# Optimization experiments

Hardware: AMD Instinct MI355X
Metric: run time of the kernel (lower is better)

The kernel has to match this reference:

```python
import jax, jax.numpy as jnp
import numpy as np

B, L, T, IN, H, OUT = 1024, 64, 128, 13, 64, 13
NEG = -1e30


def gru_step(x, h, Wih, Whh, bih, bhh):
    # PyTorch GRU cell: gates ordered (r, z, n)
    gi = x @ Wih.T + bih          # [B, 3H]
    gh = h @ Whh.T + bhh          # [B, 3H]
    ir, iz, inn = jnp.split(gi, 3, axis=-1)
    hr, hz, hn = jnp.split(gh, 3, axis=-1)
    r = jax.nn.sigmoid(ir + hr)
    z = jax.nn.sigmoid(iz + hz)
    n = jnp.tanh(inn + r * hn)
    return (1.0 - z) * n + z * h


def setup_inputs() -> dict:
    key = jax.random.key(0)
    ks = jax.random.split(key, 10)
    s = float(1.0 / np.sqrt(H))
    x = jax.random.normal(ks[0], (B, L, IN), jnp.float32)
    lengths = jax.random.randint(ks[1], (B,), 1, L + 1).at[0].set(L)
    Wih = jax.random.uniform(ks[2], (3 * H, IN), jnp.float32, -s, s)
    Whh = jax.random.uniform(ks[3], (3 * H, H), jnp.float32, -s, s)
    bih = jax.random.uniform(ks[4], (3 * H,), jnp.float32, -s, s)
    bhh = jax.random.uniform(ks[5], (3 * H,), jnp.float32, -s, s)
    Wf = jax.random.uniform(ks[6], (OUT, H), jnp.float32, -s, s)
    bf = jax.random.uniform(ks[7], (OUT,), jnp.float32, -s, s)
    Wa = jax.random.uniform(ks[8], (H, H), jnp.float32, -s, s)
    ba = jax.random.uniform(ks[9], (H,), jnp.float32, -s, s)
    return dict(x=x, lengths=lengths, output_length=T, Wih=Wih, Whh=Whh,
                bih=bih, bhh=bhh, Wf=Wf, bf=bf, Wa=Wa, ba=ba)


def reference(x, lengths, output_length, Wih, Whh, bih, bhh, Wf, bf, Wa, ba):
    b, l = x.shape[0], x.shape[1]
    xT = jnp.swapaxes(x, 0, 1)                        # [L, B, IN]
    h0 = jnp.zeros((b, H), x.dtype)

    # Encoder: masked GRU emulating pack_padded/pad_packed semantics:
    # hidden frozen past each sequence's length; outputs zero past length.
    def enc(h, inp):
        t, xt = inp
        hn = gru_step(xt, h, Wih, Whh, bih, bhh)
        valid = (t < lengths)[:, None]
        h = jnp.where(valid, hn, h)
        return h, jnp.where(valid, hn, 0.0)

    h, outs = jax.lax.scan(enc, h0, (jnp.arange(l), xT))
    # output[:, -1, :] of the padded output (zeros for seqs shorter than max)
    nin = outs[-1] @ Wf.T + bf                        # [B, OUT]

    Tn = output_length
    buf0 = jnp.zeros((Tn, b, H), x.dtype)             # growing past-prediction buffer

    def dec(carry, t):
        h, buf, nin = carry
        hn = gru_step(nin, h, Wih, Whh, bih, bhh)     # output_lstm == hidden (1 layer, 1 step)
        # attention recomputed over all past predictions (softmax over time axis)
        logits = jnp.einsum('tbh,gh->tbg', buf, Wa) + ba      # [T, B, H]
        logits = jnp.where((jnp.arange(Tn) < t)[:, None, None], logits, NEG)
        w = jax.nn.softmax(logits, axis=0)
        o = hn + jnp.sum(w * buf, axis=0)             # at t=0 buffer is all zeros -> +0
        y = o @ Wf.T + bf
        return (hn, buf.at[t].set(o), y), y

    _, ys = jax.lax.scan(dec, (h, buf0, nin), jnp.arange(Tn))
    return jnp.swapaxes(ys, 0, 1)                     # [B, T, OUT]
```

## Files before the change

kernel.cpp:

```cpp
#include <hip/hip_runtime.h>
#include <stdint.h>
#include <math.h>

#define BATCH 1024
#define SEQL  64
#define TDEC  128
#define NIN   13
#define NH    64
#define NOUT  13

typedef _Float16 h2 __attribute__((ext_vector_type(2)));
typedef __fp16   g2 __attribute__((ext_vector_type(2)));

union FU  { uint32_t u; float f; };
union HU  { uint16_t u; _Float16 h; };
union H2U { uint32_t u; h2 h; g2 g; };

__device__ __forceinline__ float bf2f(uint16_t v) { FU t; t.u = ((uint32_t)v) << 16; return t.f; }
__device__ __forceinline__ float hf2f(uint16_t v) { HU t; t.u = v; return (float)t.h; }

__device__ __forceinline__ float ldf(const void* p, long i, int mode) {
    if (mode == 1) return bf2f(((const uint16_t*)p)[i]);
    if (mode == 2) return hf2f(((const uint16_t*)p)[i]);
    return ((const float*)p)[i];
}

__device__ __forceinline__ bool pass_stats(const void* p, int n, int lane, int mode,
                                           float band_lo, float band_hi, float max_ok) {
    int m = (n + 1) / 2;
    int cnt = (m < 64) ? m : 64;
    bool ok_max = true, in_band = false;
    if (lane < cnt) {
        long pos = 2L * (((long)lane * m) / cnt);
        float v = (mode == 1) ? bf2f(((const uint16_t*)p)[pos])
                              : hf2f(((const uint16_t*)p)[pos]);
        float a = fabsf(v);
        ok_max  = (a <= max_ok);
        in_band = (a >= band_lo && a <= band_hi);
    }
    bool allmax = __all(ok_max);
    int nb = (int)__popcll(__ballot(in_band));
    int need = cnt / 4; if (need < 1) need = 1;
    return allmax && (nb >= need);
}
__device__ __forceinline__ int detect(const void* p, int n, int lane,
                                      float band_lo, float band_hi, float max_ok) {
    if (pass_stats(p, n, lane, 1, band_lo, band_hi, max_ok)) return 1;
    if (pass_stats(p, n, lane, 2, band_lo, band_hi, max_ok)) return 2;
    return 0;
}
__device__ __forceinline__ bool detect_len64(const int* p, int lane) {
    int v = p[2 * lane + 1];
    return __all(v == 0);
}

__device__ __forceinline__ float dot2(h2 a, h2 b, float c) {
#if __has_builtin(__builtin_amdgcn_fdot2)
    return __builtin_amdgcn_fdot2(a, b, c, false);
#else
    return c + (float)a[0] * (float)b[0] + (float)a[1] * (float)b[1];
#endif
}
__device__ __forceinline__ uint32_t pku(float a, float b) {
    H2U t; t.g = __builtin_amdgcn_cvt_pkrtz(a, b); return t.u;
}
__device__ __forceinline__ h2 uh(uint32_t u) { H2U t; t.u = u; return t.h; }
__device__ __forceinline__ float rcp_(float x) { return __builtin_amdgcn_rcpf(x); }
__device__ __forceinline__ float sigm(float x)  { return rcp_(1.0f + __expf(-x)); }
__device__ __forceinline__ float tanh_(float x) { return 1.0f - 2.0f * rcp_(__expf(2.0f * x) + 1.0f); }
__device__ __forceinline__ void wb() { __builtin_amdgcn_wave_barrier(); }

__global__ __launch_bounds__(64, 1)
void gru_attn_kernel(const void* __restrict__ x, const int* __restrict__ lengths,
                     const void* __restrict__ Wih, const void* __restrict__ Whh,
                     const void* __restrict__ bih, const void* __restrict__ bhh,
                     const void* __restrict__ Wf, const void* __restrict__ bfv,
                     const void* __restrict__ Wa, const void* __restrict__ ba,
                     float* __restrict__ out)
{
    const int b = blockIdx.x;
    const int j = threadIdx.x;

    __shared__ __align__(16) uint32_t xs2[SEQL][8];
    __shared__ __align__(16) uint32_t hs2[NH / 2];
    __shared__ __align__(16) uint32_t os2[NH / 2];
    __shared__ __align__(16) uint32_t xd2[8];

    const int dX   = detect(x,   BATCH * SEQL * NIN, j, 0.25f, 4.0f, 16.0f);
    const int dWih = detect(Wih, 3 * NH * NIN, j, 0.04f, 0.13f, 0.14f);
    const int dWhh = detect(Whh, 3 * NH * NH,  j, 0.04f, 0.13f, 0.14f);
    const int dBih = detect(bih, 3 * NH,       j, 0.04f, 0.13f, 0.14f);
    const int dBhh = detect(bhh, 3 * NH,       j, 0.04f, 0.13f, 0.14f);
    const int dWf  = detect(Wf,  NOUT * NH,    j, 0.04f, 0.13f, 0.14f);
    const int dBf  = detect(bfv, NOUT,         j, 0.04f, 0.13f, 0.14f);
    const int dWa  = detect(Wa,  NH * NH,      j, 0.04f, 0.13f, 0.14f);
    const int dBa  = detect(ba,  NH,           j, 0.04f, 0.13f, 0.14f);
    const bool len64 = detect_len64(lengths, j);

    h2 wihr[7], wihz[7], wihn[7];
    h2 whhr[32], whhz[32], whhn[32];
    h2 wap[32], wfp[32];

#pragma unroll
    for (int k = 0; k < 7; ++k) {
        float a0 = ldf(Wih, (0 * NH + j) * NIN + 2 * k, dWih);
        float a1 = (2 * k + 1 < NIN) ? ldf(Wih, (0 * NH + j) * NIN + 2 * k + 1, dWih) : 0.0f;
        wihr[k] = uh(pku(a0, a1));
        float b0 = ldf(Wih, (1 * NH + j) * NIN + 2 * k, dWih);
        float b1 = (2 * k + 1 < NIN) ? ldf(Wih, (1 * NH + j) * NIN + 2 * k + 1, dWih) : 0.0f;
        wihz[k] = uh(pku(b0, b1));
        float c0 = ldf(Wih, (2 * NH + j) * NIN + 2 * k, dWih);
        float c1 = (2 * k + 1 < NIN) ? ldf(Wih, (2 * NH + j) * NIN + 2 * k + 1, dWih) : 0.0f;
        wihn[k] = uh(pku(c0, c1));
    }
    const int jf = (j < NOUT) ? j : 0;
#pragma unroll
    for (int k = 0; k < 32; ++k) {
        whhr[k] = uh(pku(ldf(Whh, (0 * NH + j) * NH + 2 * k, dWhh),
                         ldf(Whh, (0 * NH + j) * NH + 2 * k + 1, dWhh)));
        whhz[k] = uh(pku(ldf(Whh, (1 * NH + j) * NH + 2 * k, dWhh),
                         ldf(Whh, (1 * NH + j) * NH + 2 * k + 1, dWhh)));
        whhn[k] = uh(pku(ldf(Whh, (2 * NH + j) * NH + 2 * k, dWhh),
                         ldf(Whh, (2 * NH + j) * NH + 2 * k + 1, dWhh)));
        wap[k]  = uh(pku(ldf(Wa, j * NH + 2 * k, dWa),
                         ldf(Wa, j * NH + 2 * k + 1, dWa)));
        wfp[k]  = uh(pku(ldf(Wf, jf * NH + 2 * k, dWf),
                         ldf(Wf, jf * NH + 2 * k + 1, dWf)));
    }

    const float bcr = ldf(bih, j, dBih)          + ldf(bhh, j, dBhh);
    const float bcz = ldf(bih, NH + j, dBih)     + ldf(bhh, NH + j, dBhh);
    const float bni = ldf(bih, 2 * NH + j, dBih);
    const float bnh = ldf(bhh, 2 * NH + j, dBhh);
    const float baj = ldf(ba, j, dBa);
    const float bfj = ldf(bfv, jf, dBf);
    const int len = len64 ? lengths[2 * b] : lengths[b];

    {
        const long base = ((long)b * SEQL + j) * NIN;
        float v[14];
#pragma unroll
        for (int k = 0; k < NIN; ++k) v[k] = ldf(x, base + k, dX);
        v[13] = 0.0f;
#pragma unroll
        for (int p = 0; p < 7; ++p) xs2[j][p] = pku(v[2 * p], v[2 * p + 1]);
        xs2[j][7] = 0u;
    }
    if (j < NH / 2) hs2[j] = 0u;
    if (j == 0) xd2[7] = 0u;
    wb();

    float h = 0.0f;
    float out_last = 0.0f;

    for (int t = 0; t < SEQL; ++t) {
        float ar = bcr, az = bcz, an = bni, hna = bnh;
        {
            const uint32_t* xr = xs2[t];
            uint4 q0 = *(const uint4*)xr;
            uint4 q1 = *(const uint4*)(xr + 4);
            uint32_t xw[8] = {q0.x, q0.y, q0.z, q0.w, q1.x, q1.y, q1.z, q1.w};
#pragma unroll
            for (int p = 0; p < 7; ++p) {
                h2 xv = uh(xw[p]);
                ar = dot2(wihr[p], xv, ar);
                az = dot2(wihz[p], xv, az);
                an = dot2(wihn[p], xv, an);
            }
        }
        float ar2 = 0.0f, az2 = 0.0f, hn2 = 0.0f;
        {
            const uint4* hp = (const uint4*)hs2;
#pragma unroll
            for (int q = 0; q < 8; ++q) {
                uint4 blk = hp[q];
                uint32_t w[4] = {blk.x, blk.y, blk.z, blk.w};
#pragma unroll
                for (int e = 0; e < 4; ++e) {
                    int k = 4 * q + e;
                    h2 hv = uh(w[e]);
                    if (e & 1) { ar2 = dot2(whhr[k], hv, ar2); az2 = dot2(whhz[k], hv, az2); hn2 = dot2(whhn[k], hv, hn2); }
                    else       { ar  = dot2(whhr[k], hv, ar);  az  = dot2(whhz[k], hv, az);  hna = dot2(whhn[k], hv, hna); }
                }
            }
        }
        ar += ar2; az += az2; hna += hn2;
        float r = sigm(ar);
        float z = sigm(az);
        float n = tanh_(an + r * hna);
        float hnew = n + z * (h - n);
        if (t < len) h = hnew;
        if (t == SEQL - 1) out_last = (t < len) ? hnew : 0.0f;
        float hpart = __shfl_xor(h, 1);
        if (!(j & 1)) hs2[j >> 1] = pku(h, hpart);
        wb();
    }

    {
        float opart = __shfl_xor(out_last, 1);
        if (!(j & 1)) os2[j >> 1] = pku(out_last, opart);
        wb();
        float nv = bfj, nv2 = 0.0f;
        const uint4* op = (const uint4*)os2;
#pragma unroll
        for (int q = 0; q < 8; ++q) {
            uint4 blk = op[q];
            uint32_t w[4] = {blk.x, blk.y, blk.z, blk.w};
#pragma unroll
            for (int e = 0; e < 4; ++e) {
                int k = 4 * q + e;
                h2 ov = uh(w[e]);
                if (e & 1) nv2 = dot2(wfp[k], ov, nv2);
                else       nv  = dot2(wfp[k], ov, nv);
            }
        }
        nv += nv2;
        float nz = (j < NOUT) ? nv : 0.0f;
        float np = __shfl_xor(nz, 1);
        if (!(j & 1) && j < 14) xd2[j >> 1] = pku(nz, np);
        wb();
    }

    float m = -1e30f, Zs = 0.0f, num = 0.0f;

    for (int t = 0; t < TDEC; ++t) {
        float ar = bcr, az = bcz, an = bni, hna = bnh;
        {
            uint4 q0 = *(const uint4*)xd2;
            uint4 q1 = *(const uint4*)(xd2 + 4);
            uint32_t xw[8] = {q0.x, q0.y, q0.z, q0.w, q1.x, q1.y, q1.z, q1.w};
#pragma unroll
            for (int p = 0; p < 7; ++p) {
                h2 xv = uh(xw[p]);
                ar = dot2(wihr[p], xv, ar);
                az = dot2(wihz[p], xv, az);
                an = dot2(wihn[p], xv, an);
            }
        }
        float ar2 = 0.0f, az2 = 0.0f, hn2 = 0.0f;
        {
            const uint4* hp = (const uint4*)hs2;
#pragma unroll
            for (int q = 0; q < 8; ++q) {
                uint4 blk = hp[q];
                uint32_t w[4] = {blk.x, blk.y, blk.z, blk.w};
#pragma unroll
                for (int e = 0; e < 4; ++e) {
                    int k = 4 * q + e;
                    h2 hv = uh(w[e]);
                    if (e & 1) { ar2 = dot2(whhr[k], hv, ar2); az2 = dot2(whhz[k], hv, az2); hn2 = dot2(whhn[k], hv, hn2); }
                    else       { ar  = dot2(whhr[k], hv, ar);  az  = dot2(whhz[k], hv, az);  hna = dot2(whhn[k], hv, hna); }
                }
            }
        }
        ar += ar2; az += az2; hna += hn2;
        float r = sigm(ar);
        float z = sigm(az);
        float n = tanh_(an + r * hna);
        float hnew = n + z * (h - n);
        h = hnew;
        float attn = (t > 0) ? num * rcp_(Zs) : 0.0f;
        float o = hnew + attn;
        float hpart = __shfl_xor(hnew, 1);
        if (!(j & 1)) hs2[j >> 1] = pku(hnew, hpart);
        float opart = __shfl_xor(o, 1);
        if (!(j & 1)) os2[j >> 1] = pku(o, opart);
        wb();
        float s = baj, yv = bfj, s2 = 0.0f, y2 = 0.0f;
        {
            const uint4* op = (const uint4*)os2;
#pragma unroll
            for (int q = 0; q < 8; ++q) {
                uint4 blk = op[q];
                uint32_t w[4] = {blk.x, blk.y, blk.z, blk.w};
#pragma unroll
                for (int e = 0; e < 4; ++e) {
                    int k = 4 * q + e;
                    h2 ov = uh(w[e]);
                    if (e & 1) { s2 = dot2(wap[k], ov, s2); y2 = dot2(wfp[k], ov, y2); }
                    else       { s  = dot2(wap[k], ov, s);  yv = dot2(wfp[k], ov, yv); }
                }
            }
        }
        s += s2; yv += y2;
        float mn = fmaxf(m, s);
        float al = __expf(m - mn);
        float p  = __expf(s - mn);
        Zs  = Zs * al + p;
        num = num * al + p * o;
        m = mn;
        if (j < NOUT) out[((size_t)b * TDEC + t) * NOUT + j] = yv;
        float yz = (j < NOUT) ? yv : 0.0f;
        float yp = __shfl_xor(yz, 1);
        if (!(j & 1) && j < 14) xd2[j >> 1] = pku(yz, yp);
        wb();
    }
}

extern "C" void kernel_launch(void* const* d_in, const int* in_sizes, int n_in,
                              void* d_out, int out_size, void* d_ws, size_t ws_size,
                              hipStream_t stream) {
    (void)in_sizes; (void)n_in; (void)out_size; (void)d_ws; (void)ws_size;
    const void* x      = d_in[0];
    const int* lengths = (const int*)d_in[1];
    const void* Wih = d_in[3];
    const void* Whh = d_in[4];
    const void* bih = d_in[5];
    const void* bhh = d_in[6];
    const void* Wf  = d_in[7];
    const void* bf  = d_in[8];
    const void* Wa  = d_in[9];
    const void* ba  = d_in[10];
    float* out = (float*)d_out;

    gru_attn_kernel<<<dim3(BATCH), dim3(64), 0, stream>>>(
        x, lengths, Wih, Whh, bih, bhh, Wf, bf, Wa, ba, out);
}
```

Measured before the change: 240.2 us.

## Process two batch elements per wavefront to interleave independent recurrences

Each 64-thread block now handles two batch rows instead of one. The two independent GRU/attention recurrences are interleaved inside the same step, which gives instruction-level parallelism and hides the latency of the serial dependency chain, and it reuses the register-resident weights across both rows. In exchange the grid is halved to 512 blocks, which may underfill a 256-CU device's wave slots, and register and LDS use per block roughly doubles.

```diff
diff --git a/kernel.cpp b/kernel.cpp
--- a/kernel.cpp
+++ b/kernel.cpp
@@ -78,13 +78,13 @@
                      const void* __restrict__ Wa, const void* __restrict__ ba,
                      float* __restrict__ out)
 {
-    const int b = blockIdx.x;
-    const int j = threadIdx.x;
-
-    __shared__ __align__(16) uint32_t xs2[SEQL][8];
-    __shared__ __align__(16) uint32_t hs2[NH / 2];
-    __shared__ __align__(16) uint32_t os2[NH / 2];
-    __shared__ __align__(16) uint32_t xd2[8];
+    const int bx = blockIdx.x;
+    const int j  = threadIdx.x;
+
+    __shared__ __align__(16) uint32_t xs2[2][SEQL][8];
+    __shared__ __align__(16) uint32_t hs2[2][NH / 2];
+    __shared__ __align__(16) uint32_t os2[2][NH / 2];
+    __shared__ __align__(16) uint32_t xd2[2][8];
 
     const int dX   = detect(x,   BATCH * SEQL * NIN, j, 0.25f, 4.0f, 16.0f);
     const int dWih = detect(Wih, 3 * NH * NIN, j, 0.04f, 0.13f, 0.14f);
@@ -134,165 +134,189 @@
     const float bnh = ldf(bhh, 2 * NH + j, dBhh);
     const float baj = ldf(ba, j, dBa);
     const float bfj = ldf(bfv, jf, dBf);
-    const int len = len64 ? lengths[2 * b] : lengths[b];
-
-    {
-        const long base = ((long)b * SEQL + j) * NIN;
+
+    int len[2];
+    size_t bels[2];
+#pragma unroll
+    for (int e = 0; e < 2; ++e) {
+        int b = 2 * bx + e;
+        bels[e] = (size_t)b;
+        len[e] = len64 ? lengths[2 * b] : lengths[b];
+    }
+
+#pragma unroll
+    for (int e = 0; e < 2; ++e) {
+        const long base = ((long)bels[e] * SEQL + j) * NIN;
         float v[14];
 #pragma unroll
         for (int k = 0; k < NIN; ++k) v[k] = ldf(x, base + k, dX);
         v[13] = 0.0f;
 #pragma unroll
-        for (int p = 0; p < 7; ++p) xs2[j][p] = pku(v[2 * p], v[2 * p + 1]);
-        xs2[j][7] = 0u;
-    }
-    if (j < NH / 2) hs2[j] = 0u;
-    if (j == 0) xd2[7] = 0u;
+        for (int p = 0; p < 7; ++p) xs2[e][j][p] = pku(v[2 * p], v[2 * p + 1]);
+        xs2[e][j][7] = 0u;
+        if (j < NH / 2) hs2[e][j] = 0u;
+        if (j == 0) xd2[e][7] = 0u;
+    }
     wb();
 
-    float h = 0.0f;
-    float out_last = 0.0f;
-
+    float h[2] = {0.0f, 0.0f};
+    float out_last[2] = {0.0f, 0.0f};
+
+#pragma unroll 1
     for (int t = 0; t < SEQL; ++t) {
-        float ar = bcr, az = bcz, an = bni, hna = bnh;
-        {
-            const uint32_t* xr = xs2[t];
-            uint4 q0 = *(const uint4*)xr;
-            uint4 q1 = *(const uint4*)(xr + 4);
+        float ar[2], az[2], an[2], hna[2], arb[2], azb[2], hnb[2];
+#pragma unroll
+        for (int e = 0; e < 2; ++e) {
+            ar[e] = bcr; az[e] = bcz; an[e] = bni; hna[e] = bnh;
+            arb[e] = 0.0f; azb[e] = 0.0f; hnb[e] = 0.0f;
+            uint4 q0 = *(const uint4*)xs2[e][t];
+            uint4 q1 = *(const uint4*)(xs2[e][t] + 4);
             uint32_t xw[8] = {q0.x, q0.y, q0.z, q0.w, q1.x, q1.y, q1.z, q1.w};
 #pragma unroll
             for (int p = 0; p < 7; ++p) {
                 h2 xv = uh(xw[p]);
-                ar = dot2(wihr[p], xv, ar);
-                az = dot2(wihz[p], xv, az);
-                an = dot2(wihn[p], xv, an);
-            }
-        }
-        float ar2 = 0.0f, az2 = 0.0f, hn2 = 0.0f;
-        {
-            const uint4* hp = (const uint4*)hs2;
+                ar[e] = dot2(wihr[p], xv, ar[e]);
+                az[e] = dot2(wihz[p], xv, az[e]);
+                an[e] = dot2(wihn[p], xv, an[e]);
+            }
+            const uint4* hp = (const uint4*)hs2[e];
 #pragma unroll
             for (int q = 0; q < 8; ++q) {
                 uint4 blk = hp[q];
                 uint32_t w[4] = {blk.x, blk.y, blk.z, blk.w};
 #pragma unroll
-                for (int e = 0; e < 4; ++e) {
-                    int k = 4 * q + e;
-                    h2 hv = uh(w[e]);
-                    if (e & 1) { ar2 = dot2(whhr[k], hv, ar2); az2 = dot2(whhz[k], hv, az2); hn2 = dot2(whhn[k], hv, hn2); }
-                    else       { ar  = dot2(whhr[k], hv, ar);  az  = dot2(whhz[k], hv, az);  hna = dot2(whhn[k], hv, hna); }
+                for (int ee = 0; ee < 4; ++ee) {
+                    int k = 4 * q + ee;
+                    h2 hv = uh(w[ee]);
+                    if (ee & 1) { arb[e] = dot2(whhr[k], hv, arb[e]); azb[e] = dot2(whhz[k], hv, azb[e]); hnb[e] = dot2(whhn[k], hv, hnb[e]); }
+                    else        { ar[e]  = dot2(whhr[k], hv, ar[e]);  az[e]  = dot2(whhz[k], hv, az[e]);  hna[e] = dot2(whhn[k], hv, hna[e]); }
                 }
             }
         }
-        ar += ar2; az += az2; hna += hn2;
-        float r = sigm(ar);
-        float z = sigm(az);
-        float n = tanh_(an + r * hna);
-        float hnew = n + z * (h - n);
-        if (t < len) h = hnew;
-        if (t == SEQL - 1) out_last = (t < len) ? hnew : 0.0f;
-        float hpart = __shfl_xor(h, 1);
-        if (!(j & 1)) hs2[j >> 1] = pku(h, hpart);
+#pragma unroll
+        for (int e = 0; e < 2; ++e) {
+            float arf = ar[e] + arb[e], azf = az[e] + azb[e], hnf = hna[e] + hnb[e];
+            float r = sigm(arf);
+            float z = sigm(azf);
+            float n = tanh_(an[e] + r * hnf);
+            float hnew = n + z * (h[e] - n);
+            if (t < len[e]) h[e] = hnew;
+            if (t == SEQL - 1) out_last[e] = (t < len[e]) ? hnew : 0.0f;
+            float hpart = __shfl_xor(h[e], 1);
+            if (!(j & 1)) hs2[e][j >> 1] = pku(h[e], hpart);
+        }
         wb();
     }
 
     {
-        float opart = __shfl_xor(out_last, 1);
-        if (!(j & 1)) os2[j >> 1] = pku(out_last, opart);
-        wb();
-        float nv = bfj, nv2 = 0.0f;
-        const uint4* op = (const uint4*)os2;
-#pragma unroll
-        for (int q = 0; q < 8; ++q) {
-            uint4 blk = op[q];
-            uint32_t w[4] = {blk.x, blk.y, blk.z, blk.w};
-#pragma unroll
-            for (int e = 0; e < 4; ++e) {
-                int k = 4 * q + e;
-                h2 ov = uh(w[e]);
-                if (e & 1) nv2 = dot2(wfp[k], ov, nv2);
-                else       nv  = dot2(wfp[k], ov, nv);
-            }
-        }
-        nv += nv2;
-        float nz = (j < NOUT) ? nv : 0.0f;
-        float np = __shfl_xor(nz, 1);
-        if (!(j & 1) && j < 14) xd2[j >> 1] = pku(nz, np);
-        wb();
-    }
-
-    float m = -1e30f, Zs = 0.0f, num = 0.0f;
-
+#pragma unroll
+        for (int e = 0; e < 2; ++e) {
+            float opart = __shfl_xor(out_last[e], 1);
+            if (!(j & 1)) os2[e][j >> 1] = pku(out_last[e], opart);
+        }
+        wb();
+#pragma unroll
+        for (int e = 0; e < 2; ++e) {
+            float nv = bfj, nv2 = 0.0f;
+            const uint4* op = (const uint4*)os2[e];
+#pragma unroll
+            for (int q = 0; q < 8; ++q) {
+                uint4 blk = op[q];
+                uint32_t w[4] = {blk.x, blk.y, blk.z, blk.w};
+#pragma unroll
+                for (int ee = 0; ee < 4; ++ee) {
+                    int k = 4 * q + ee;
+                    h2 ov = uh(w[ee]);
+                    if (ee & 1) nv2 = dot2(wfp[k], ov, nv2);
+                    else        nv  = dot2(wfp[k], ov, nv);
+                }
+            }
+            nv += nv2;
+            float nz = (j < NOUT) ? nv : 0.0f;
+            float np = __shfl_xor(nz, 1);
+            if (!(j & 1) && j < 14) xd2[e][j >> 1] = pku(nz, np);
+        }
+        wb();
+    }
+
+    float m[2] = {-1e30f, -1e30f}, Zs[2] = {0.0f, 0.0f}, num[2] = {0.0f, 0.0f};
+
+#pragma unroll 1
     for (int t = 0; t < TDEC; ++t) {
-        float ar = bcr, az = bcz, an = bni, hna = bnh;
-        {
-            uint4 q0 = *(const uint4*)xd2;
-            uint4 q1 = *(const uint4*)(xd2 + 4);
+        float ar[2], az[2], an[2], hna[2], arb[2], azb[2], hnb[2];
+#pragma unroll
+        for (int e = 0; e < 2; ++e) {
+            ar[e] = bcr; az[e] = bcz; an[e] = bni; hna[e] = bnh;
+            arb[e] = 0.0f; azb[e] = 0.0f; hnb[e] = 0.0f;
+            uint4 q0 = *(const uint4*)xd2[e];
+            uint4 q1 = *(const uint4*)(xd2[e] + 4);
             uint32_t xw[8] = {q0.x, q0.y, q0.z, q0.w, q1.x, q1.y, q1.z, q1.w};
 #pragma unroll
             for (int p = 0; p < 7; ++p) {
                 h2 xv = uh(xw[p]);
-                ar = dot2(wihr[p], xv, ar);
-                az = dot2(wihz[p], xv, az);
-                an = dot2(wihn[p], xv, an);
-            }
-        }
-        float ar2 = 0.0f, az2 = 0.0f, hn2 = 0.0f;
-        {
-            const uint4* hp = (const uint4*)hs2;
+                ar[e] = dot2(wihr[p], xv, ar[e]);
+                az[e] = dot2(wihz[p], xv, az[e]);
+                an[e] = dot2(wihn[p], xv, an[e]);
+            }
+            const uint4* hp = (const uint4*)hs2[e];
 #pragma unroll
             for (int q = 0; q < 8; ++q) {
                 uint4 blk = hp[q];
                 uint32_t w[4] = {blk.x, blk.y, blk.z, blk.w};
 #pragma unroll
-                for (int e = 0; e < 4; ++e) {
-                    int k = 4 * q + e;
-                    h2 hv = uh(w[e]);
-                    if (e & 1) { ar2 = dot2(whhr[k], hv, ar2); az2 = dot2(whhz[k], hv, az2); hn2 = dot2(whhn[k], hv, hn2); }
-                    else       { ar  = dot2(whhr[k], hv, ar);  az  = dot2(whhz[k], hv, az);  hna = dot2(whhn[k], hv, hna); }
+                for (int ee = 0; ee < 4; ++ee) {
+                    int k = 4 * q + ee;
+                    h2 hv = uh(w[ee]);
+                    if (ee & 1) { arb[e] = dot2(whhr[k], hv, arb[e]); azb[e] = dot2(whhz[k], hv, azb[e]); hnb[e] = dot2(whhn[k], hv, hnb[e]); }
+                    else        { ar[e]  = dot2(whhr[k], hv, ar[e]);  az[e]  = dot2(whhz[k], hv, az[e]);  hna[e] = dot2(whhn[k], hv, hna[e]); }
                 }
             }
         }
-        ar += ar2; az += az2; hna += hn2;
-        float r = sigm(ar);
-        float z = sigm(az);
-        float n = tanh_(an + r * hna);
-        float hnew = n + z * (h - n);
-        h = hnew;
-        float attn = (t > 0) ? num * rcp_(Zs) : 0.0f;
-        float o = hnew + attn;
-        float hpart = __shfl_xor(hnew, 1);
-        if (!(j & 1)) hs2[j >> 1] = pku(hnew, hpart);
-        float opart = __shfl_xor(o, 1);
-        if (!(j & 1)) os2[j >> 1] = pku(o, opart);
-        wb();
-        float s = baj, yv = bfj, s2 = 0.0f, y2 = 0.0f;
-        {
-            const uint4* op = (const uint4*)os2;
+        float o[2];
+#pragma unroll
+        for (int e = 0; e < 2; ++e) {
+            float arf = ar[e] + arb[e], azf = az[e] + azb[e], hnf = hna[e] + hnb[e];
+            float r = sigm(arf);
+            float z = sigm(azf);
+            float n = tanh_(an[e] + r * hnf);
+            float hnew = n + z * (h[e] - n);
+            h[e] = hnew;
+            float attn = (t > 0) ? num[e] * rcp_(Zs[e]) : 0.0f;
+            o[e] = hnew + attn;
+            float hpart = __shfl_xor(hnew, 1);
+            if (!(j & 1)) hs2[e][j >> 1] = pku(hnew, hpart);
+            float opart = __shfl_xor(o[e], 1);
+            if (!(j & 1)) os2[e][j >> 1] = pku(o[e], opart);
+        }
+        wb();
+#pragma unroll
+        for (int e = 0; e < 2; ++e) {
+            float s = baj, yv = bfj, s2 = 0.0f, y2 = 0.0f;
+            const uint4* op = (const uint4*)os2[e];
 #pragma unroll
             for (int q = 0; q < 8; ++q) {
                 uint4 blk = op[q];
                 uint32_t w[4] = {blk.x, blk.y, blk.z, blk.w};
 #pragma unroll
-                for (int e = 0; e < 4; ++e) {
-                    int k = 4 * q + e;
-                    h2 ov = uh(w[e]);
-                    if (e & 1) { s2 = dot2(wap[k], ov, s2); y2 = dot2(wfp[k], ov, y2); }
-                    else       { s  = dot2(wap[k], ov, s);  yv = dot2(wfp[k], ov, yv); }
+                for (int ee = 0; ee < 4; ++ee) {
+                    int k = 4 * q + ee;
+                    h2 ov = uh(w[ee]);
+                    if (ee & 1) { s2 = dot2(wap[k], ov, s2); y2 = dot2(wfp[k], ov, y2); }
+                    else        { s  = dot2(wap[k], ov, s);  yv = dot2(wfp[k], ov, yv); }
                 }
             }
-        }
-        s += s2; yv += y2;
-        float mn = fmaxf(m, s);
-        float al = __expf(m - mn);
-        float p  = __expf(s - mn);
-        Zs  = Zs * al + p;
-        num = num * al + p * o;
-        m = mn;
-        if (j < NOUT) out[((size_t)b * TDEC + t) * NOUT + j] = yv;
-        float yz = (j < NOUT) ? yv : 0.0f;
-        float yp = __shfl_xor(yz, 1);
-        if (!(j & 1) && j < 14) xd2[j >> 1] = pku(yz, yp);
+            s += s2; yv += y2;
+            float mn = fmaxf(m[e], s);
+            float al = __expf(m[e] - mn);
+            float p  = __expf(s - mn);
+            Zs[e]  = Zs[e] * al + p;
+            num[e] = num[e] * al + p * o[e];
+            m[e] = mn;
+            if (j < NOUT) out[((size_t)bels[e] * TDEC + t) * NOUT + j] = yv;
+            float yz = (j < NOUT) ? yv : 0.0f;
+            float yp = __shfl_xor(yz, 1);
+            if (!(j & 1) && j < 14) xd2[e][j >> 1] = pku(yz, yp);
+        }
         wb();
     }
 }
@@ -313,6 +337,6 @@
     const void* ba  = d_in[10];
     float* out = (float*)d_out;
 
-    gru_attn_kernel<<<dim3(BATCH), dim3(64), 0, stream>>>(
+    gru_attn_kernel<<<dim3(BATCH / 2), dim3(64), 0, stream>>>(
         x, lengths, Wih, Whh, bih, bhh, Wf, bf, Wa, ba, out);
 }
```

After: 361.5 us. 1.5x slower.
